# Performance work log

Hardware: AMD Instinct MI355X
Metric: run time of the kernel (lower is better)

## Reference

```python
import jax, jax.numpy as jnp
import numpy as np

EPS = 1e-6

def _phi(x):
    # elu_feature_map: elu(x) + 1 (positive feature map)
    return jax.nn.elu(x) + 1.0

def setup_inputs() -> dict:
    key = jax.random.key(0)
    ks = jax.random.split(key, 6)
    N, L, S, H, E, D = 4, 2048, 2048, 16, 64, 64
    return {
        "queries1": jax.random.normal(ks[0], (N, L, H, E), jnp.float32),
        "keys1": jax.random.normal(ks[1], (N, S, H, E), jnp.float32),
        "values1": jax.random.normal(ks[2], (N, S, H, D), jnp.float32),
        "queries2": jax.random.normal(ks[3], (N, L, H, E), jnp.float32),
        "keys2": jax.random.normal(ks[4], (N, S, H, E), jnp.float32),
        "values2": jax.random.normal(ks[5], (N, S, H, D), jnp.float32),
        "key_lengths1": jnp.ones((N, S), jnp.float32),
        "key_lengths2": jnp.ones((N, S), jnp.float32),
    }

def _linear_cross(Q, K_other, V_other):
    # Q: (N,L,H,E) featurized queries; K_other: (N,S,H,E) featurized+masked keys
    # KV: (N,H,D,E) ; 'nshd,nshm->nhmd'
    KV = jnp.einsum('nshd,nshm->nhmd', K_other, V_other)
    Ksum = K_other.sum(axis=1)                      # (N,H,E)
    Z = 1.0 / (jnp.einsum('nlhd,nhd->nlh', Q, Ksum) + EPS)
    # 'nlhd,nhmd,nlh->nlhm'
    return jnp.einsum('nlhd,nhmd->nlhm', Q, KV) * Z[..., None]

def reference(queries1, keys1, values1, queries2, keys2, values2,
              key_lengths1, key_lengths2):
    Q1 = _phi(queries1)
    K1 = _phi(keys1) * key_lengths1[:, :, None, None]
    Q2 = _phi(queries2)
    K2 = _phi(keys2) * key_lengths2[:, :, None, None]
    V1 = _linear_cross(Q1, K2, values2)  # stream1 queries attend to stream2 keys/values
    V2 = _linear_cross(Q2, K1, values1)  # stream2 queries attend to stream1 keys/values
    return (V1, V2)
```

## Files before the change

### kernel.cpp

```cpp
#include <hip/hip_runtime.h>

#define NB 4
#define LL 2048
#define SS 2048
#define HH 16
#define EE 64
#define DD 64

#define KVTOT (2*NB*HH*4096)
#define WSFLOATS (KVTOT + 2*NB*HH*64)

__device__ inline float phi(float x) { return x > 0.f ? x + 1.f : __expf(x); }

__global__ __launch_bounds__(256) void kv_kernel(
    const float* __restrict__ k1, const float* __restrict__ v1,
    const float* __restrict__ k2, const float* __restrict__ v2,
    const float* __restrict__ kl1, const float* __restrict__ kl2,
    float* __restrict__ ws)
{
    const int b = blockIdx.x;
    const int chunk = b & 7;
    const int h = (b >> 3) & 15;
    const int n = (b >> 7) & 3;
    const int st = (b >> 9) & 1;
    const float* K  = st == 0 ? k2 : k1;
    const float* V  = st == 0 ? v2 : v1;
    const float* KL = st == 0 ? kl2 : kl1;

    const int t = threadIdx.x;
    __shared__ float Kl[16][68];
    __shared__ float Vl[16][68];

    const int r  = t >> 4;
    const int c4 = (t & 15) * 4;
    const int d0 = (t >> 4) * 4;
    const int m0 = (t & 15) * 4;

    float acc[4][4];
#pragma unroll
    for (int i = 0; i < 4; i++)
#pragma unroll
        for (int j = 0; j < 4; j++) acc[i][j] = 0.f;
    float ks = 0.f;

    const int sbase = chunk * 256;
    for (int stage = 0; stage < 16; stage++) {
        __syncthreads();
        {
            const int s = sbase + stage * 16 + r;
            const size_t rowoff = ((size_t)(((size_t)n * SS + s) * HH + h)) * EE;
            float4 kf = *reinterpret_cast<const float4*>(&K[rowoff + c4]);
            float4 vf = *reinterpret_cast<const float4*>(&V[rowoff + c4]);
            const float kl = KL[(size_t)n * SS + s];
            Kl[r][c4 + 0] = phi(kf.x) * kl;
            Kl[r][c4 + 1] = phi(kf.y) * kl;
            Kl[r][c4 + 2] = phi(kf.z) * kl;
            Kl[r][c4 + 3] = phi(kf.w) * kl;
            Vl[r][c4 + 0] = vf.x;
            Vl[r][c4 + 1] = vf.y;
            Vl[r][c4 + 2] = vf.z;
            Vl[r][c4 + 3] = vf.w;
        }
        __syncthreads();
#pragma unroll
        for (int s2 = 0; s2 < 16; s2++) {
            float4 kk = *reinterpret_cast<const float4*>(&Kl[s2][d0]);
            float4 vv = *reinterpret_cast<const float4*>(&Vl[s2][m0]);
            float ka[4] = {kk.x, kk.y, kk.z, kk.w};
            float va[4] = {vv.x, vv.y, vv.z, vv.w};
#pragma unroll
            for (int i = 0; i < 4; i++)
#pragma unroll
                for (int j = 0; j < 4; j++) acc[i][j] += ka[i] * va[j];
        }
        if (t < 64) {
#pragma unroll
            for (int s2 = 0; s2 < 16; s2++) ks += Kl[s2][t];
        }
    }

    const size_t kvbase = ((size_t)((st * NB + n) * HH + h)) * 4096;
#pragma unroll
    for (int i = 0; i < 4; i++)
#pragma unroll
        for (int j = 0; j < 4; j++)
            atomicAdd(&ws[kvbase + (size_t)(d0 + i) * 64 + (m0 + j)], acc[i][j]);
    if (t < 64)
        atomicAdd(&ws[KVTOT + ((size_t)(st * NB + n) * HH + h) * 64 + t], ks);
}

__global__ __launch_bounds__(256) void out_kernel(
    const float* __restrict__ q1, const float* __restrict__ q2,
    const float* __restrict__ ws, float* __restrict__ out)
{
    const int b = blockIdx.x;
    const int lc = b & 15;
    const int h = (b >> 4) & 15;
    const int n = (b >> 8) & 3;
    const int st = (b >> 10) & 1;
    const float* Q = st == 0 ? q1 : q2;
    const size_t outoff = (size_t)st * ((size_t)NB * LL * HH * DD);

    __shared__ float T[4096];
    __shared__ float Qt[64][132];
    __shared__ float Zl[128];
    __shared__ float Ks[64];

    const int t = threadIdx.x;
    const size_t kvbase = ((size_t)((st * NB + n) * HH + h)) * 4096;
#pragma unroll
    for (int i = 0; i < 16; i++) T[i * 256 + t] = ws[kvbase + i * 256 + t];
    if (t < 64) Ks[t] = ws[KVTOT + ((size_t)(st * NB + n) * HH + h) * 64 + t];

    {
        const int l = t >> 1;
        const int dd0 = (t & 1) * 32;
        const int lg = lc * 128 + l;
        const size_t qoff = ((size_t)(((size_t)n * LL + lg) * HH + h)) * EE + dd0;
#pragma unroll
        for (int i = 0; i < 8; i++) {
            float4 qu = *reinterpret_cast<const float4*>(&Q[qoff + i * 4]);
            const int db = dd0 + i * 4;
            Qt[db + 0][l] = phi(qu.x);
            Qt[db + 1][l] = phi(qu.y);
            Qt[db + 2][l] = phi(qu.z);
            Qt[db + 3][l] = phi(qu.w);
        }
    }
    __syncthreads();

    if (t < 128) {
        float z = 0.f;
#pragma unroll
        for (int d = 0; d < 64; d++) z += Qt[d][t] * Ks[d];
        Zl[t] = 1.f / (z + 1e-6f);
    }
    __syncthreads();

    const int m0 = (t & 15) * 4;
    const int l0 = (t >> 4) * 8;
    float acc[8][4];
#pragma unroll
    for (int i = 0; i < 8; i++)
#pragma unroll
        for (int j = 0; j < 4; j++) acc[i][j] = 0.f;

    for (int d = 0; d < 64; d++) {
        float4 tv = *reinterpret_cast<const float4*>(&T[d * 64 + m0]);
        float4 qa = *reinterpret_cast<const float4*>(&Qt[d][l0]);
        float4 qb = *reinterpret_cast<const float4*>(&Qt[d][l0 + 4]);
        float tm[4] = {tv.x, tv.y, tv.z, tv.w};
        float ql[8] = {qa.x, qa.y, qa.z, qa.w, qb.x, qb.y, qb.z, qb.w};
#pragma unroll
        for (int i = 0; i < 8; i++)
#pragma unroll
            for (int j = 0; j < 4; j++) acc[i][j] += ql[i] * tm[j];
    }

#pragma unroll
    for (int i = 0; i < 8; i++) {
        const int l = l0 + i;
        const int lg = lc * 128 + l;
        const float z = Zl[l];
        float4 o;
        o.x = acc[i][0] * z;
        o.y = acc[i][1] * z;
        o.z = acc[i][2] * z;
        o.w = acc[i][3] * z;
        *reinterpret_cast<float4*>(
            &out[outoff + ((size_t)(((size_t)n * LL + lg) * HH + h)) * DD + m0]) = o;
    }
}

extern "C" void kernel_launch(void* const* d_in, const int* in_sizes, int n_in,
                              void* d_out, int out_size, void* d_ws, size_t ws_size,
                              hipStream_t stream) {
    const float* q1  = (const float*)d_in[0];
    const float* k1  = (const float*)d_in[1];
    const float* v1  = (const float*)d_in[2];
    const float* q2  = (const float*)d_in[3];
    const float* k2  = (const float*)d_in[4];
    const float* v2  = (const float*)d_in[5];
    const float* kl1 = (const float*)d_in[6];
    const float* kl2 = (const float*)d_in[7];
    float* ws = (float*)d_ws;
    float* out = (float*)d_out;

    hipMemsetAsync(d_ws, 0, (size_t)WSFLOATS * sizeof(float), stream);
    kv_kernel<<<dim3(1024), dim3(256), 0, stream>>>(k1, v1, k2, v2, kl1, kl2, ws);
    out_kernel<<<dim3(2048), dim3(256), 0, stream>>>(q1, q2, ws, out);
}
```

Baseline: 291.4 us.

## Use split-bf16 MFMA for KV and output contractions with register prefetch

After: 253.9 us. 1.15x faster.

```diff
diff --git a/kernel.cpp b/kernel.cpp
--- a/kernel.cpp
+++ b/kernel.cpp
@@ -10,7 +10,22 @@
 #define KVTOT (2*NB*HH*4096)
 #define WSFLOATS (KVTOT + 2*NB*HH*64)
 
+typedef short short8 __attribute__((ext_vector_type(8)));
+typedef float floatx4 __attribute__((ext_vector_type(4)));
+
 __device__ inline float phi(float x) { return x > 0.f ? x + 1.f : __expf(x); }
+
+__device__ inline unsigned int f2bf(float f) {
+    unsigned int x = __float_as_uint(f);
+    return (x + 0x7FFFu + ((x >> 16) & 1u)) >> 16;
+}
+__device__ inline void split_pack(float a, float b, unsigned int &hp, unsigned int &lp) {
+    const unsigned int ha = f2bf(a), hb = f2bf(b);
+    const float ra = a - __uint_as_float(ha << 16);
+    const float rb = b - __uint_as_float(hb << 16);
+    hp = (ha & 0xFFFFu) | (hb << 16);
+    lp = (f2bf(ra) & 0xFFFFu) | (f2bf(rb) << 16);
+}
 
 __global__ __launch_bounds__(256) void kv_kernel(
     const float* __restrict__ k1, const float* __restrict__ v1,
@@ -23,70 +38,134 @@
     const int h = (b >> 3) & 15;
     const int n = (b >> 7) & 3;
     const int st = (b >> 9) & 1;
-    const float* K  = st == 0 ? k2 : k1;
-    const float* V  = st == 0 ? v2 : v1;
-    const float* KL = st == 0 ? kl2 : kl1;
+    const float* K  = st ? k1 : k2;
+    const float* V  = st ? v1 : v2;
+    const float* KL = st ? kl1 : kl2;
+
+    __shared__ __align__(16) unsigned short KtH[64][72];
+    __shared__ __align__(16) unsigned short KtL[64][72];
+    __shared__ __align__(16) unsigned short VtH[64][72];
+    __shared__ __align__(16) unsigned short VtL[64][72];
 
     const int t = threadIdx.x;
-    __shared__ float Kl[16][68];
-    __shared__ float Vl[16][68];
-
-    const int r  = t >> 4;
-    const int c4 = (t & 15) * 4;
-    const int d0 = (t >> 4) * 4;
-    const int m0 = (t & 15) * 4;
-
-    float acc[4][4];
-#pragma unroll
-    for (int i = 0; i < 4; i++)
-#pragma unroll
-        for (int j = 0; j < 4; j++) acc[i][j] = 0.f;
-    float ks = 0.f;
-
-    const int sbase = chunk * 256;
-    for (int stage = 0; stage < 16; stage++) {
+    const int lane = t & 63;
+    const int w = t >> 6;
+    const int d4 = t & 15;
+    const int sp = t >> 4;
+    const int c = lane & 15;
+    const int q = lane >> 4;
+
+    float ksum[4] = {0.f, 0.f, 0.f, 0.f};
+    floatx4 acc[4];
+#pragma unroll
+    for (int i = 0; i < 4; i++) acc[i] = (floatx4){0.f, 0.f, 0.f, 0.f};
+
+    float4 cur[8]; float curl[4];
+    {
+        const int sbase = chunk * 256;
+#pragma unroll
+        for (int i = 0; i < 2; ++i) {
+            const int sl = 2 * sp + 32 * i;
+            const size_t off = ((size_t)((size_t)n * SS + sbase + sl) * HH + h) * EE + 4 * d4;
+            cur[4 * i + 0] = *(const float4*)&K[off];
+            cur[4 * i + 1] = *(const float4*)&K[off + HH * EE];
+            cur[4 * i + 2] = *(const float4*)&V[off];
+            cur[4 * i + 3] = *(const float4*)&V[off + HH * EE];
+            curl[2 * i + 0] = KL[(size_t)n * SS + sbase + sl];
+            curl[2 * i + 1] = KL[(size_t)n * SS + sbase + sl + 1];
+        }
+    }
+
+    for (int g = 0; g < 4; ++g) {
+        float4 nxt[8]; float nxtl[4];
+        if (g < 3) {
+            const int sbase = chunk * 256 + (g + 1) * 64;
+#pragma unroll
+            for (int i = 0; i < 2; ++i) {
+                const int sl = 2 * sp + 32 * i;
+                const size_t off = ((size_t)((size_t)n * SS + sbase + sl) * HH + h) * EE + 4 * d4;
+                nxt[4 * i + 0] = *(const float4*)&K[off];
+                nxt[4 * i + 1] = *(const float4*)&K[off + HH * EE];
+                nxt[4 * i + 2] = *(const float4*)&V[off];
+                nxt[4 * i + 3] = *(const float4*)&V[off + HH * EE];
+                nxtl[2 * i + 0] = KL[(size_t)n * SS + sbase + sl];
+                nxtl[2 * i + 1] = KL[(size_t)n * SS + sbase + sl + 1];
+            }
+        }
+        if (g) __syncthreads();
+#pragma unroll
+        for (int i = 0; i < 2; ++i) {
+            const int sl = 2 * sp + 32 * i;
+            const float4 ka = cur[4 * i + 0], kb = cur[4 * i + 1];
+            const float4 va = cur[4 * i + 2], vb = cur[4 * i + 3];
+            const float l0 = curl[2 * i + 0], l1 = curl[2 * i + 1];
+            const float a0 = phi(ka.x) * l0, a1 = phi(ka.y) * l0;
+            const float a2 = phi(ka.z) * l0, a3 = phi(ka.w) * l0;
+            const float b0 = phi(kb.x) * l1, b1 = phi(kb.y) * l1;
+            const float b2 = phi(kb.z) * l1, b3 = phi(kb.w) * l1;
+            ksum[0] += a0 + b0; ksum[1] += a1 + b1;
+            ksum[2] += a2 + b2; ksum[3] += a3 + b3;
+            unsigned int hp, lp;
+            split_pack(a0, b0, hp, lp);
+            *(unsigned int*)&KtH[4 * d4 + 0][sl] = hp; *(unsigned int*)&KtL[4 * d4 + 0][sl] = lp;
+            split_pack(a1, b1, hp, lp);
+            *(unsigned int*)&KtH[4 * d4 + 1][sl] = hp; *(unsigned int*)&KtL[4 * d4 + 1][sl] = lp;
+            split_pack(a2, b2, hp, lp);
+            *(unsigned int*)&KtH[4 * d4 + 2][sl] = hp; *(unsigned int*)&KtL[4 * d4 + 2][sl] = lp;
+            split_pack(a3, b3, hp, lp);
+            *(unsigned int*)&KtH[4 * d4 + 3][sl] = hp; *(unsigned int*)&KtL[4 * d4 + 3][sl] = lp;
+            split_pack(va.x, vb.x, hp, lp);
+            *(unsigned int*)&VtH[4 * d4 + 0][sl] = hp; *(unsigned int*)&VtL[4 * d4 + 0][sl] = lp;
+            split_pack(va.y, vb.y, hp, lp);
+            *(unsigned int*)&VtH[4 * d4 + 1][sl] = hp; *(unsigned int*)&VtL[4 * d4 + 1][sl] = lp;
+            split_pack(va.z, vb.z, hp, lp);
+            *(unsigned int*)&VtH[4 * d4 + 2][sl] = hp; *(unsigned int*)&VtL[4 * d4 + 2][sl] = lp;
+            split_pack(va.w, vb.w, hp, lp);
+            *(unsigned int*)&VtH[4 * d4 + 3][sl] = hp; *(unsigned int*)&VtL[4 * d4 + 3][sl] = lp;
+        }
         __syncthreads();
-        {
-            const int s = sbase + stage * 16 + r;
-            const size_t rowoff = ((size_t)(((size_t)n * SS + s) * HH + h)) * EE;
-            float4 kf = *reinterpret_cast<const float4*>(&K[rowoff + c4]);
-            float4 vf = *reinterpret_cast<const float4*>(&V[rowoff + c4]);
-            const float kl = KL[(size_t)n * SS + s];
-            Kl[r][c4 + 0] = phi(kf.x) * kl;
-            Kl[r][c4 + 1] = phi(kf.y) * kl;
-            Kl[r][c4 + 2] = phi(kf.z) * kl;
-            Kl[r][c4 + 3] = phi(kf.w) * kl;
-            Vl[r][c4 + 0] = vf.x;
-            Vl[r][c4 + 1] = vf.y;
-            Vl[r][c4 + 2] = vf.z;
-            Vl[r][c4 + 3] = vf.w;
-        }
-        __syncthreads();
-#pragma unroll
-        for (int s2 = 0; s2 < 16; s2++) {
-            float4 kk = *reinterpret_cast<const float4*>(&Kl[s2][d0]);
-            float4 vv = *reinterpret_cast<const float4*>(&Vl[s2][m0]);
-            float ka[4] = {kk.x, kk.y, kk.z, kk.w};
-            float va[4] = {vv.x, vv.y, vv.z, vv.w};
-#pragma unroll
-            for (int i = 0; i < 4; i++)
-#pragma unroll
-                for (int j = 0; j < 4; j++) acc[i][j] += ka[i] * va[j];
-        }
-        if (t < 64) {
-#pragma unroll
-            for (int s2 = 0; s2 < 16; s2++) ks += Kl[s2][t];
+#pragma unroll
+        for (int ks = 0; ks < 2; ++ks) {
+            const short8 aH = *(const short8*)&VtH[16 * w + c][32 * ks + 8 * q];
+            const short8 aL = *(const short8*)&VtL[16 * w + c][32 * ks + 8 * q];
+#pragma unroll
+            for (int dt = 0; dt < 4; ++dt) {
+                const short8 bH = *(const short8*)&KtH[16 * dt + c][32 * ks + 8 * q];
+                const short8 bL = *(const short8*)&KtL[16 * dt + c][32 * ks + 8 * q];
+                acc[dt] = __builtin_amdgcn_mfma_f32_16x16x32_bf16(aH, bH, acc[dt], 0, 0, 0);
+                acc[dt] = __builtin_amdgcn_mfma_f32_16x16x32_bf16(aH, bL, acc[dt], 0, 0, 0);
+                acc[dt] = __builtin_amdgcn_mfma_f32_16x16x32_bf16(aL, bH, acc[dt], 0, 0, 0);
+            }
+        }
+        if (g < 3) {
+#pragma unroll
+            for (int i = 0; i < 8; ++i) cur[i] = nxt[i];
+#pragma unroll
+            for (int i = 0; i < 4; ++i) curl[i] = nxtl[i];
         }
     }
 
     const size_t kvbase = ((size_t)((st * NB + n) * HH + h)) * 4096;
 #pragma unroll
-    for (int i = 0; i < 4; i++)
-#pragma unroll
-        for (int j = 0; j < 4; j++)
-            atomicAdd(&ws[kvbase + (size_t)(d0 + i) * 64 + (m0 + j)], acc[i][j]);
-    if (t < 64)
-        atomicAdd(&ws[KVTOT + ((size_t)(st * NB + n) * HH + h) * 64 + t], ks);
+    for (int dt = 0; dt < 4; ++dt)
+#pragma unroll
+        for (int r = 0; r < 4; ++r)
+            atomicAdd(&ws[kvbase + (size_t)(16 * w + 4 * q + r) * 64 + 16 * dt + c],
+                      acc[dt][r]);
+
+    float (*scr)[64] = (float(*)[64])VtL;
+    __syncthreads();
+    scr[sp][4 * d4 + 0] = ksum[0];
+    scr[sp][4 * d4 + 1] = ksum[1];
+    scr[sp][4 * d4 + 2] = ksum[2];
+    scr[sp][4 * d4 + 3] = ksum[3];
+    __syncthreads();
+    if (t < 64) {
+        float s = 0.f;
+#pragma unroll
+        for (int i = 0; i < 16; ++i) s += scr[i][t];
+        atomicAdd(&ws[KVTOT + ((size_t)(st * NB + n) * HH + h) * 64 + t], s);
+    }
 }
 
 __global__ __launch_bounds__(256) void out_kernel(
@@ -94,81 +173,111 @@
     const float* __restrict__ ws, float* __restrict__ out)
 {
     const int b = blockIdx.x;
-    const int lc = b & 15;
-    const int h = (b >> 4) & 15;
-    const int n = (b >> 8) & 3;
-    const int st = (b >> 10) & 1;
-    const float* Q = st == 0 ? q1 : q2;
-    const size_t outoff = (size_t)st * ((size_t)NB * LL * HH * DD);
-
-    __shared__ float T[4096];
-    __shared__ float Qt[64][132];
-    __shared__ float Zl[128];
+    const int lc = b & 7;
+    const int h = (b >> 3) & 15;
+    const int n = (b >> 7) & 3;
+    const int st = (b >> 9) & 1;
+    const float* Q = st ? q2 : q1;
+    float* O = out + (size_t)st * ((size_t)NB * LL * HH * DD);
+
+    __shared__ __align__(16) unsigned short BtH[64][72];
+    __shared__ __align__(16) unsigned short BtL[64][72];
     __shared__ float Ks[64];
+    __shared__ float Zl[256];
 
     const int t = threadIdx.x;
+    const int lane = t & 63;
+    const int w = t >> 6;
+    const int c = lane & 15;
+    const int q = lane >> 4;
     const size_t kvbase = ((size_t)((st * NB + n) * HH + h)) * 4096;
-#pragma unroll
-    for (int i = 0; i < 16; i++) T[i * 256 + t] = ws[kvbase + i * 256 + t];
+
+    {
+        const int m = t >> 2;
+        const int dbase = (t & 3) * 16;
+#pragma unroll
+        for (int i = 0; i < 4; ++i) {
+            const int d0 = dbase + 4 * i;
+            const float4 kv = *(const float4*)&ws[kvbase + (size_t)m * 64 + d0];
+            unsigned int hp, lp;
+            split_pack(kv.x, kv.y, hp, lp);
+            *(unsigned int*)&BtH[m][d0]     = hp; *(unsigned int*)&BtL[m][d0]     = lp;
+            split_pack(kv.z, kv.w, hp, lp);
+            *(unsigned int*)&BtH[m][d0 + 2] = hp; *(unsigned int*)&BtL[m][d0 + 2] = lp;
+        }
+    }
     if (t < 64) Ks[t] = ws[KVTOT + ((size_t)(st * NB + n) * HH + h) * 64 + t];
+    __syncthreads();
+
+    const int lbase = lc * 256;
 
     {
-        const int l = t >> 1;
-        const int dd0 = (t & 1) * 32;
-        const int lg = lc * 128 + l;
-        const size_t qoff = ((size_t)(((size_t)n * LL + lg) * HH + h)) * EE + dd0;
-#pragma unroll
-        for (int i = 0; i < 8; i++) {
-            float4 qu = *reinterpret_cast<const float4*>(&Q[qoff + i * 4]);
-            const int db = dd0 + i * 4;
-            Qt[db + 0][l] = phi(qu.x);
-            Qt[db + 1][l] = phi(qu.y);
-            Qt[db + 2][l] = phi(qu.z);
-            Qt[db + 3][l] = phi(qu.w);
-        }
-    }
+        const float* qr = &Q[((size_t)((size_t)n * LL + lbase + t) * HH + h) * EE];
+        float z = 0.f;
+#pragma unroll
+        for (int d = 0; d < 64; d += 4) {
+            const float4 qv = *(const float4*)&qr[d];
+            z += phi(qv.x) * Ks[d] + phi(qv.y) * Ks[d + 1]
+               + phi(qv.z) * Ks[d + 2] + phi(qv.w) * Ks[d + 3];
+        }
+        Zl[t] = 1.f / (z + 1e-6f);
+    }
+
+    short8 bH[8], bL[8];
+#pragma unroll
+    for (int mt = 0; mt < 4; ++mt)
+#pragma unroll
+        for (int ks = 0; ks < 2; ++ks) {
+            bH[2 * mt + ks] = *(const short8*)&BtH[16 * mt + c][32 * ks + 8 * q];
+            bL[2 * mt + ks] = *(const short8*)&BtL[16 * mt + c][32 * ks + 8 * q];
+        }
     __syncthreads();
 
-    if (t < 128) {
-        float z = 0.f;
-#pragma unroll
-        for (int d = 0; d < 64; d++) z += Qt[d][t] * Ks[d];
-        Zl[t] = 1.f / (z + 1e-6f);
-    }
-    __syncthreads();
-
-    const int m0 = (t & 15) * 4;
-    const int l0 = (t >> 4) * 8;
-    float acc[8][4];
-#pragma unroll
-    for (int i = 0; i < 8; i++)
-#pragma unroll
-        for (int j = 0; j < 4; j++) acc[i][j] = 0.f;
-
-    for (int d = 0; d < 64; d++) {
-        float4 tv = *reinterpret_cast<const float4*>(&T[d * 64 + m0]);
-        float4 qa = *reinterpret_cast<const float4*>(&Qt[d][l0]);
-        float4 qb = *reinterpret_cast<const float4*>(&Qt[d][l0 + 4]);
-        float tm[4] = {tv.x, tv.y, tv.z, tv.w};
-        float ql[8] = {qa.x, qa.y, qa.z, qa.w, qb.x, qb.y, qb.z, qb.w};
-#pragma unroll
-        for (int i = 0; i < 8; i++)
-#pragma unroll
-            for (int j = 0; j < 4; j++) acc[i][j] += ql[i] * tm[j];
-    }
-
-#pragma unroll
-    for (int i = 0; i < 8; i++) {
-        const int l = l0 + i;
-        const int lg = lc * 128 + l;
-        const float z = Zl[l];
-        float4 o;
-        o.x = acc[i][0] * z;
-        o.y = acc[i][1] * z;
-        o.z = acc[i][2] * z;
-        o.w = acc[i][3] * z;
-        *reinterpret_cast<float4*>(
-            &out[outoff + ((size_t)(((size_t)n * LL + lg) * HH + h)) * DD + m0]) = o;
+    floatx4 acc[16];
+#pragma unroll
+    for (int i = 0; i < 16; ++i) acc[i] = (floatx4){0.f, 0.f, 0.f, 0.f};
+
+#pragma unroll
+    for (int lt = 0; lt < 4; ++lt) {
+        const int l = lbase + 64 * w + 16 * lt + c;
+        const float* qr = &Q[((size_t)((size_t)n * LL + l) * HH + h) * EE];
+#pragma unroll
+        for (int ks = 0; ks < 2; ++ks) {
+            const int d0 = 32 * ks + 8 * q;
+            const float4 qa = *(const float4*)&qr[d0];
+            const float4 qb = *(const float4*)&qr[d0 + 4];
+            const float p[8] = {phi(qa.x), phi(qa.y), phi(qa.z), phi(qa.w),
+                                phi(qb.x), phi(qb.y), phi(qb.z), phi(qb.w)};
+            short8 aH, aL;
+#pragma unroll
+            for (int j = 0; j < 8; ++j) {
+                const unsigned int hb = f2bf(p[j]);
+                aH[j] = (short)hb;
+                aL[j] = (short)f2bf(p[j] - __uint_as_float(hb << 16));
+            }
+#pragma unroll
+            for (int mt = 0; mt < 4; ++mt) {
+                acc[4 * lt + mt] = __builtin_amdgcn_mfma_f32_16x16x32_bf16(
+                    aH, bH[2 * mt + ks], acc[4 * lt + mt], 0, 0, 0);
+                acc[4 * lt + mt] = __builtin_amdgcn_mfma_f32_16x16x32_bf16(
+                    aH, bL[2 * mt + ks], acc[4 * lt + mt], 0, 0, 0);
+                acc[4 * lt + mt] = __builtin_amdgcn_mfma_f32_16x16x32_bf16(
+                    aL, bH[2 * mt + ks], acc[4 * lt + mt], 0, 0, 0);
+            }
+        }
+    }
+
+#pragma unroll
+    for (int lt = 0; lt < 4; ++lt) {
+#pragma unroll
+        for (int r = 0; r < 4; ++r) {
+            const int ll = 64 * w + 16 * lt + 4 * q + r;
+            const float z = Zl[ll];
+            const size_t ro = ((size_t)((size_t)n * LL + lbase + ll) * HH + h) * DD;
+#pragma unroll
+            for (int mt = 0; mt < 4; ++mt)
+                O[ro + 16 * mt + c] = acc[4 * lt + mt][r] * z;
+        }
     }
 }
 
@@ -188,5 +297,5 @@
 
     hipMemsetAsync(d_ws, 0, (size_t)WSFLOATS * sizeof(float), stream);
     kv_kernel<<<dim3(1024), dim3(256), 0, stream>>>(k1, v1, k2, v2, kl1, kl2, ws);
-    out_kernel<<<dim3(2048), dim3(256), 0, stream>>>(q1, q2, ws, out);
-}
+    out_kernel<<<dim3(1024), dim3(256), 0, stream>>>(q1, q2, ws, out);
+}
```
